# Optimization experiments

Measured on AMD Instinct MI355X. Metric: run time of the kernel, lower is better.

## Reference

```python
import jax, jax.numpy as jnp
import numpy as np

SELF_DIM = 6   # self_state_dim
HID = 50       # lstm_hidden_dim


def setup_inputs() -> dict:
    key = jax.random.key(0)
    ks = jax.random.split(key, 16)
    B, N, D = 8192, 64, 13  # batch, num humans, joint-state length

    def w(k, shape):
        # kaiming-ish init, stored as [in, out] so forward is x @ W + b
        return jax.random.normal(k, shape, jnp.float32) / jnp.sqrt(jnp.float32(shape[0]))

    z = lambda n: jnp.zeros((n,), jnp.float32)
    return {
        "state": jax.random.normal(ks[0], (B, N, D), jnp.float32),
        # mlp1: 13 -> 150 -> 100, last_relu=True
        "mlp1_w1": w(ks[1], (13, 150)),  "mlp1_b1": z(150),
        "mlp1_w2": w(ks[2], (150, 100)), "mlp1_b2": z(100),
        # attention: 200 -> 100 -> 100 -> 1 (no relu on last)
        "attn_w1": w(ks[3], (200, 100)), "attn_b1": z(100),
        "attn_w2": w(ks[4], (100, 100)), "attn_b2": z(100),
        "attn_w3": w(ks[5], (100, 1)),   "attn_b3": z(1),
        # LSTM(input=7, hidden=50), torch gate order i,f,g,o
        "lstm_wih": w(ks[6], (7, 4 * HID)),
        "lstm_whh": w(ks[7], (HID, 4 * HID)),
        "lstm_bih": z(4 * HID), "lstm_bhh": z(4 * HID),
        # mlp: 56 -> 150 -> 100 -> 100 -> 1
        "mlp_w1": w(ks[8], (SELF_DIM + HID, 150)), "mlp_b1": z(150),
        "mlp_w2": w(ks[9], (150, 100)),            "mlp_b2": z(100),
        "mlp_w3": w(ks[10], (100, 100)),           "mlp_b3": z(100),
        "mlp_w4": w(ks[11], (100, 1)),             "mlp_b4": z(1),
    }


def reference(state, mlp1_w1, mlp1_b1, mlp1_w2, mlp1_b2,
              attn_w1, attn_b1, attn_w2, attn_b2, attn_w3, attn_b3,
              lstm_wih, lstm_whh, lstm_bih, lstm_bhh,
              mlp_w1, mlp_b1, mlp_w2, mlp_b2, mlp_w3, mlp_b3, mlp_w4, mlp_b4):
    relu = jax.nn.relu
    B, N, D = state.shape
    self_state = state[:, 0, :SELF_DIM]      # [B, 6]
    human_state = state[:, :, SELF_DIM:]     # [B, N, 7]

    # mlp1 over all B*N per-human joint-state rows (last_relu=True)
    flat = state.reshape(B * N, D)
    m1 = relu(relu(flat @ mlp1_w1 + mlp1_b1) @ mlp1_w2 + mlp1_b2)   # [B*N, 100]

    # mean-pooled global state, broadcast back per human, concat, attention score
    gdim = m1.shape[-1]
    global_state = jnp.mean(m1.reshape(B, N, gdim), axis=1, keepdims=True)
    global_state = jnp.broadcast_to(global_state, (B, N, gdim)).reshape(B * N, gdim)
    a_in = jnp.concatenate([m1, global_state], axis=1)               # [B*N, 200]
    scores = (relu(relu(a_in @ attn_w1 + attn_b1) @ attn_w2 + attn_b2) @ attn_w3 + attn_b3)
    scores = scores.reshape(B, N)
    # NOTE: in the original torch code `scores` only feed `rerank_human_state`,
    # which is never consumed (dead code) -- the LSTM runs on the UNSORTED
    # human_state. We keep the score computation for fidelity; the per-sample
    # argsort/gather is dropped since it does not affect the output.

    # LSTM over the N humans (batch_first in torch, h0=c0=0)
    xs = jnp.transpose(human_state, (1, 0, 2))   # [N, B, 7]
    h0 = jnp.zeros((B, HID), state.dtype)

    def step(carry, x_t):
        h, c = carry
        gates = x_t @ lstm_wih + h @ lstm_whh + lstm_bih + lstm_bhh  # [B, 4H]
        i, f, g, o = jnp.split(gates, 4, axis=-1)
        c = jax.nn.sigmoid(f) * c + jax.nn.sigmoid(i) * jnp.tanh(g)
        h = jax.nn.sigmoid(o) * jnp.tanh(c)
        return (h, c), None

    (hn, _cn), _ = jax.lax.scan(step, (h0, h0), xs)

    # value head on [self_state, h_n]
    joint = jnp.concatenate([self_state, hn], axis=1)   # [B, 56]
    x = relu(joint @ mlp_w1 + mlp_b1)
    x = relu(x @ mlp_w2 + mlp_b2)
    x = relu(x @ mlp_w3 + mlp_b3)
    value = x @ mlp_w4 + mlp_b4                          # [B, 1]
    return value
```

## Files before the change

### kernel.cpp

```cpp
#include <hip/hip_runtime.h>

typedef __attribute__((ext_vector_type(8))) short short8;
typedef __attribute__((ext_vector_type(4))) float f32x4;
union frag_u { short8 v; unsigned short u[8]; };

__device__ __forceinline__ float bf2f(unsigned short b) {
  unsigned int u = ((unsigned int)b) << 16;
  float f; __builtin_memcpy(&f, &u, 4); return f;
}
__device__ __forceinline__ unsigned short f2bf(float f) {
  unsigned int u; __builtin_memcpy(&u, &f, 4);
  return (unsigned short)((u + 0x7FFFu + ((u >> 16) & 1u)) >> 16);
}
__device__ __forceinline__ unsigned short hi_of(float f) { return f2bf(f); }
__device__ __forceinline__ unsigned short lo_of(float f) {
  unsigned short h = f2bf(f); return f2bf(f - bf2f(h));
}
__device__ __forceinline__ float sigm(float x) {
  return __builtin_amdgcn_rcpf(1.f + __expf(-x));
}
__device__ __forceinline__ float tanh_(float x) {
  return 1.f - 2.f * __builtin_amdgcn_rcpf(1.f + __expf(2.f * x));
}

__global__ void detect_dtype_kernel(const unsigned short* s, int* flag) {
  int i = threadIdx.x;
  unsigned short v = s[2 * i];
  int e = (v >> 7) & 0xFF;
  unsigned long long m = __ballot(e < 100 || e > 140);
  if (i == 0) *flag = (__popcll(m) >= 16) ? 1 : 0;
}

template <int AS, typename GetB, typename GetW>
__device__ __forceinline__ void mfma_layer(const unsigned short* sA, float* sG,
    int wave, int col, int quad, int kc_n, int ntiles, int N, GetB getb, GetW getw)
{
  for (int tile = wave; tile < ntiles; tile += 16) {
    int n = tile * 16 + col;
    float b = (n < N) ? getb(n) : 0.f;
    f32x4 acc = {b, b, b, b};
    for (int kc = 0; kc < kc_n; ++kc) {
      short8 a = *(const short8*)&sA[col * AS + kc * 32 + quad * 8];
      frag_u w;
      #pragma unroll
      for (int j = 0; j < 8; ++j) {
        int k = kc * 32 + quad * 8 + j;
        w.u[j] = (n < N) ? getw(k, n) : (unsigned short)0;
      }
      acc = __builtin_amdgcn_mfma_f32_16x16x32_bf16(a, w.v, acc, 0, 0, 0);
    }
    *(f32x4*)&sG[n * 20 + quad * 4] = acc;
  }
}

template <int AS, bool LO>
__device__ __forceinline__ void relu_fill(const float* sG, unsigned short* sA,
                                          int tid, int N, int loOff, int Kpad) {
  for (int idx = tid; idx < 16 * Kpad; idx += 1024) {
    int m = idx & 15, n = idx >> 4;
    unsigned short v = 0;
    if (n < N) {
      v = f2bf(fmaxf(sG[n * 20 + m], 0.f));
    } else if (LO && n >= loOff && n < loOff + N) {
      float x = fmaxf(sG[(n - loOff) * 20 + m], 0.f);
      v = lo_of(x);
    }
    sA[m * AS + n] = v;
  }
}

template <bool F32>
__global__ __launch_bounds__(1024, 8) void value_net_kernel(
    const void* state_, const void* wih_, const void* whh_,
    const void* bih_, const void* bhh_,
    const void* w1_, const void* b1_, const void* w2_, const void* b2_,
    const void* w3_, const void* b3_, const void* w4_, const void* b4_,
    void* out_, const int* flag)
{
  if (flag && *flag != (F32 ? 1 : 0)) return;

  constexpr int AS = F32 ? 328 : 168;
  constexpr int KC = F32 ? 6 : 4;

  __shared__ __align__(16) unsigned short sA[2][16 * AS];
  __shared__ __align__(16) float sG[208 * 20];

  const unsigned short* st16 = (const unsigned short*)state_;
  const float*          stf  = (const float*)state_;

  const int tid  = threadIdx.x;
  const int wave = tid >> 6;
  const int lane = tid & 63;
  const int col  = lane & 15;
  const int quad = lane >> 4;
  const int r0   = blockIdx.x * 16;

  {
    unsigned int* a32 = (unsigned int*)&sA[0][0];
    constexpr int ZT = 16 * AS;
    #pragma unroll
    for (int i = 0; i < (ZT + 1023) / 1024; ++i) {
      int idx = tid + i * 1024;
      if (idx < ZT) a32[idx] = 0;
    }
  }

  auto W_lstm = [&](int k, int n) -> unsigned short {
    if constexpr (!F32) {
      const unsigned short* wih = (const unsigned short*)wih_;
      const unsigned short* whh = (const unsigned short*)whh_;
      if (k < 7)   return wih[k * 200 + n];
      if (k < 57)  return whh[(k - 7) * 200 + n];
      if (k < 107) return whh[(k - 57) * 200 + n];
      return (unsigned short)0;
    } else {
      const float* wih = (const float*)wih_;
      const float* whh = (const float*)whh_;
      if (k < 7)   return hi_of(wih[k * 200 + n]);
      if (k < 14)  return hi_of(wih[(k - 7) * 200 + n]);
      if (k < 21)  return lo_of(wih[(k - 14) * 200 + n]);
      if (k < 71)  return hi_of(whh[(k - 21) * 200 + n]);
      if (k < 121) return hi_of(whh[(k - 71) * 200 + n]);
      if (k < 171) return lo_of(whh[(k - 121) * 200 + n]);
      return (unsigned short)0;
    }
  };
  auto ldf = [&](const void* p, int i) -> float {
    if constexpr (F32) return ((const float*)p)[i];
    else               return bf2f(((const unsigned short*)p)[i]);
  };

  const bool hasTile = (wave < 13);
  frag_u wf[KC];
  float  wb = 0.f;
  if (hasTile) {
    int nn = wave * 16 + col;
    int no = (nn < 200) ? ((nn & 3) * 50 + (nn >> 2)) : 0;
    #pragma unroll
    for (int kc = 0; kc < KC; ++kc) {
      #pragma unroll
      for (int j = 0; j < 8; ++j) {
        int k = kc * 32 + quad * 8 + j;
        wf[kc].u[j] = (nn < 200) ? W_lstm(k, no) : (unsigned short)0;
      }
    }
    wb = (nn < 200) ? (ldf(bih_, no) + ldf(bhh_, no)) : 0.f;
  }

  const int  u_   = wave * 4 + quad;
  const bool iact = hasTile && (u_ < 50);
  float c_ = 0.f, hf = 0.f;

  const bool isx = (tid >= 832) && (tid < 944);
  const int  xm = (tid - 832) / 7, xd = (tid - 832) - ((tid - 832) / 7) * 7;
  auto xgidx = [&](int t) -> size_t { return (size_t)(r0 + xm) * 832 + t * 13 + 6 + xd; };
  auto xwrite = [&](unsigned short* sAw, float fv, unsigned short bv) {
    if constexpr (!F32) { sAw[xm * AS + xd] = bv; }
    else {
      unsigned short h = f2bf(fv);
      sAw[xm * AS + xd] = h; sAw[xm * AS + 14 + xd] = h;
      sAw[xm * AS + 7 + xd] = f2bf(fv - bf2f(h));
    }
  };
  unsigned short xv16 = 0; float xvf = 0.f;

  __syncthreads();
  if (isx) {
    if constexpr (!F32) { xwrite(&sA[0][0], 0.f, st16[xgidx(0)]); xv16 = st16[xgidx(1)]; }
    else                { xwrite(&sA[0][0], stf[xgidx(0)], 0);    xvf  = stf[xgidx(1)]; }
  }
  __syncthreads();

  for (int t = 0; t < 64; ++t) {
    const unsigned short* sAr = &sA[t & 1][0];
    unsigned short*       sAw = &sA[(t & 1) ^ 1][0];

    if (hasTile) {
      short8 a[KC];
      #pragma unroll
      for (int kc = 0; kc < KC; ++kc)
        a[kc] = *(const short8*)&sAr[col * AS + kc * 32 + quad * 8];
      f32x4 acc = {wb, wb, wb, wb};
      #pragma unroll
      for (int kc = 0; kc < KC; ++kc)
        acc = __builtin_amdgcn_mfma_f32_16x16x32_bf16(a[kc], wf[kc].v, acc, 0, 0, 0);
      *(f32x4*)&sG[(wave * 16 + col) * 20 + quad * 4] = acc;

      if (iact) {
        int nb = (wave * 16 + quad * 4);
        float gi = sG[(nb + 0) * 20 + col];
        float gf = sG[(nb + 1) * 20 + col];
        float gg = sG[(nb + 2) * 20 + col];
        float go = sG[(nb + 3) * 20 + col];
        float cc = sigm(gf) * c_ + sigm(gi) * tanh_(gg);
        c_ = cc;
        float h = sigm(go) * tanh_(cc);
        if (t < 63) {
          unsigned short hb = f2bf(h);
          unsigned short hl = f2bf(h - bf2f(hb));
          if constexpr (!F32) {
            sAw[col * AS + 7 + u_] = hb; sAw[col * AS + 57 + u_] = hl;
          } else {
            sAw[col * AS + 21 + u_] = hb; sAw[col * AS + 121 + u_] = hb;
            sAw[col * AS + 71 + u_] = hl;
          }
        } else hf = h;
      }
    } else if (isx && t < 63) {
      if constexpr (!F32) xwrite(sAw, 0.f, xv16); else xwrite(sAw, xvf, 0);
      if (t < 62) { if constexpr (!F32) xv16 = st16[xgidx(t + 2)]; else xvf = stf[xgidx(t + 2)]; }
    }
    __syncthreads();
  }

  unsigned short* sA0 = &sA[0][0];
  {
    constexpr int Z0 = F32 ? 112 : 104;
    constexpr int Z1 = F32 ? 192 : 128;
    for (int idx = tid; idx < 16 * (Z1 - Z0); idx += 1024) {
      int m = idx & 15, n = Z0 + (idx >> 4);
      sA0[m * AS + n] = 0;
    }
  }
  __syncthreads();
  if (iact) {
    unsigned short hb = f2bf(hf);
    unsigned short hl = f2bf(hf - bf2f(hb));
    sA0[col * AS + 6 + u_] = hb;
    if constexpr (!F32) sA0[col * AS + 56 + u_] = hl; else sA0[col * AS + 62 + u_] = hl;
  }
  if (tid < 96) {
    int m = tid / 6, d = tid - (tid / 6) * 6;
    if constexpr (!F32) sA0[m * AS + d] = st16[(size_t)(r0 + m) * 832 + d];
    else {
      float f = stf[(size_t)(r0 + m) * 832 + d];
      sA0[m * AS + d] = hi_of(f); sA0[m * AS + 56 + d] = lo_of(f);
    }
  }
  __syncthreads();

  mfma_layer<AS>(sA0, sG, wave, col, quad, 4, 10, 150,
    [&](int n) { return ldf(b1_, n); },
    [&](int k, int n) -> unsigned short {
      if constexpr (!F32) {
        const unsigned short* w1 = (const unsigned short*)w1_;
        if (k < 56)  return w1[k * 150 + n];
        if (k < 106) return w1[(k - 50) * 150 + n];
        return (unsigned short)0;
      } else {
        const float* w1 = (const float*)w1_;
        if (k < 56)  return hi_of(w1[k * 150 + n]);
        if (k < 112) return hi_of(w1[(k - 56) * 150 + n]);
        return (unsigned short)0;
      }
    });
  __syncthreads();
  if constexpr (!F32) relu_fill<AS, false>(sG, sA0, tid, 150, 160, 160);
  else                relu_fill<AS, true >(sG, sA0, tid, 150, 150, 320);
  __syncthreads();

  mfma_layer<AS>(sA0, sG, wave, col, quad, F32 ? 10 : 5, 7, 100,
    [&](int n) { return ldf(b2_, n); },
    [&](int k, int n) -> unsigned short {
      if constexpr (!F32) {
        const unsigned short* w2 = (const unsigned short*)w2_;
        return (k < 150) ? w2[k * 100 + n] : (unsigned short)0;
      } else {
        const float* w2 = (const float*)w2_;
        if (k < 150) return hi_of(w2[k * 100 + n]);
        if (k < 300) return hi_of(w2[(k - 150) * 100 + n]);
        return (unsigned short)0;
      }
    });
  __syncthreads();
  if constexpr (!F32) relu_fill<AS, false>(sG, sA0, tid, 100, 128, 128);
  else                relu_fill<AS, true >(sG, sA0, tid, 100, 100, 224);
  __syncthreads();

  mfma_layer<AS>(sA0, sG, wave, col, quad, F32 ? 7 : 4, 7, 100,
    [&](int n) { return ldf(b3_, n); },
    [&](int k, int n) -> unsigned short {
      if constexpr (!F32) {
        const unsigned short* w3 = (const unsigned short*)w3_;
        return (k < 100) ? w3[k * 100 + n] : (unsigned short)0;
      } else {
        const float* w3 = (const float*)w3_;
        if (k < 100) return hi_of(w3[k * 100 + n]);
        if (k < 200) return hi_of(w3[(k - 100) * 100 + n]);
        return (unsigned short)0;
      }
    });
  __syncthreads();

  if (tid < 256) {
    int m = tid >> 4, j0 = tid & 15;
    float s = 0.f;
    for (int j = j0; j < 100; j += 16)
      s += fmaxf(sG[j * 20 + m], 0.f) * ldf(w4_, j);
    s += __shfl_xor(s, 8); s += __shfl_xor(s, 4);
    s += __shfl_xor(s, 2); s += __shfl_xor(s, 1);
    if (j0 == 0) {
      float v = s + ldf(b4_, 0);
      if constexpr (!F32) ((unsigned short*)out_)[r0 + m] = f2bf(v);
      else                ((float*)out_)[r0 + m] = v;
    }
  }
}

extern "C" void kernel_launch(void* const* d_in, const int* in_sizes, int n_in,
                              void* d_out, int out_size, void* d_ws, size_t ws_size,
                              hipStream_t stream) {
  (void)n_in; (void)out_size;
  const void* state = d_in[0];
  const void* wih = d_in[11]; const void* whh = d_in[12];
  const void* bih = d_in[13]; const void* bhh = d_in[14];
  const void* w1  = d_in[15]; const void* b1  = d_in[16];
  const void* w2  = d_in[17]; const void* b2  = d_in[18];
  const void* w3  = d_in[19]; const void* b3  = d_in[20];
  const void* w4  = d_in[21]; const void* b4  = d_in[22];

  const long long F32B  = 8192LL * 64 * 13 * 4;
  const long long BF16B = 8192LL * 64 * 13 * 2;
  long long sz = in_sizes ? (long long)in_sizes[0] : -1;

  if (sz == F32B) {
    value_net_kernel<true><<<dim3(512), dim3(1024), 0, stream>>>(
        state, wih, whh, bih, bhh, w1, b1, w2, b2, w3, b3, w4, b4, d_out,
        (const int*)nullptr);
  } else if (sz == BF16B) {
    value_net_kernel<false><<<dim3(512), dim3(1024), 0, stream>>>(
        state, wih, whh, bih, bhh, w1, b1, w2, b2, w3, b3, w4, b4, d_out,
        (const int*)nullptr);
  } else if (ws_size >= sizeof(int)) {
    int* flag = (int*)d_ws;
    detect_dtype_kernel<<<dim3(1), dim3(64), 0, stream>>>(
        (const unsigned short*)state, flag);
    value_net_kernel<false><<<dim3(512), dim3(1024), 0, stream>>>(
        state, wih, whh, bih, bhh, w1, b1, w2, b2, w3, b3, w4, b4, d_out, flag);
    value_net_kernel<true><<<dim3(512), dim3(1024), 0, stream>>>(
        state, wih, whh, bih, bhh, w1, b1, w2, b2, w3, b3, w4, b4, d_out, flag);
  } else {
    value_net_kernel<false><<<dim3(512), dim3(1024), 0, stream>>>(
        state, wih, whh, bih, bhh, w1, b1, w2, b2, w3, b3, w4, b4, d_out,
        (const int*)nullptr);
  }
}
```

Baseline: 232.8 us.

## Collapse each block to a single wave running all LSTM gate tiles without barriers

Each block shrinks from 1024 threads to one 64-lane wave. That wave holds all 13 LSTM weight tiles in registers and runs every gate tile and cell update for its 16 rows itself. This removes the per-timestep __syncthreads and the separate input-loader threads; x prefetch and the MLP head now run inside the same wave. The trade-off is that one wave serialises about 13 times more MFMA and activation work per step. Only 512 waves run across the whole GPU, and register pressure rises sharply from the 13xKC weight fragments.

```diff
diff --git a/kernel.cpp b/kernel.cpp
--- a/kernel.cpp
+++ b/kernel.cpp
@@ -31,46 +31,8 @@
   if (i == 0) *flag = (__popcll(m) >= 16) ? 1 : 0;
 }
 
-template <int AS, typename GetB, typename GetW>
-__device__ __forceinline__ void mfma_layer(const unsigned short* sA, float* sG,
-    int wave, int col, int quad, int kc_n, int ntiles, int N, GetB getb, GetW getw)
-{
-  for (int tile = wave; tile < ntiles; tile += 16) {
-    int n = tile * 16 + col;
-    float b = (n < N) ? getb(n) : 0.f;
-    f32x4 acc = {b, b, b, b};
-    for (int kc = 0; kc < kc_n; ++kc) {
-      short8 a = *(const short8*)&sA[col * AS + kc * 32 + quad * 8];
-      frag_u w;
-      #pragma unroll
-      for (int j = 0; j < 8; ++j) {
-        int k = kc * 32 + quad * 8 + j;
-        w.u[j] = (n < N) ? getw(k, n) : (unsigned short)0;
-      }
-      acc = __builtin_amdgcn_mfma_f32_16x16x32_bf16(a, w.v, acc, 0, 0, 0);
-    }
-    *(f32x4*)&sG[n * 20 + quad * 4] = acc;
-  }
-}
-
-template <int AS, bool LO>
-__device__ __forceinline__ void relu_fill(const float* sG, unsigned short* sA,
-                                          int tid, int N, int loOff, int Kpad) {
-  for (int idx = tid; idx < 16 * Kpad; idx += 1024) {
-    int m = idx & 15, n = idx >> 4;
-    unsigned short v = 0;
-    if (n < N) {
-      v = f2bf(fmaxf(sG[n * 20 + m], 0.f));
-    } else if (LO && n >= loOff && n < loOff + N) {
-      float x = fmaxf(sG[(n - loOff) * 20 + m], 0.f);
-      v = lo_of(x);
-    }
-    sA[m * AS + n] = v;
-  }
-}
-
 template <bool F32>
-__global__ __launch_bounds__(1024, 8) void value_net_kernel(
+__global__ __launch_bounds__(64, 1) void value_net_kernel(
     const void* state_, const void* wih_, const void* whh_,
     const void* bih_, const void* bhh_,
     const void* w1_, const void* b1_, const void* w2_, const void* b2_,
@@ -88,21 +50,14 @@
   const unsigned short* st16 = (const unsigned short*)state_;
   const float*          stf  = (const float*)state_;
 
-  const int tid  = threadIdx.x;
-  const int wave = tid >> 6;
-  const int lane = tid & 63;
+  const int lane = threadIdx.x;
   const int col  = lane & 15;
   const int quad = lane >> 4;
   const int r0   = blockIdx.x * 16;
 
   {
     unsigned int* a32 = (unsigned int*)&sA[0][0];
-    constexpr int ZT = 16 * AS;
-    #pragma unroll
-    for (int i = 0; i < (ZT + 1023) / 1024; ++i) {
-      int idx = tid + i * 1024;
-      if (idx < ZT) a32[idx] = 0;
-    }
+    for (int idx = lane; idx < 16 * AS; idx += 64) a32[idx] = 0;
   }
 
   auto W_lstm = [&](int k, int n) -> unsigned short {
@@ -130,31 +85,34 @@
     else               return bf2f(((const unsigned short*)p)[i]);
   };
 
-  const bool hasTile = (wave < 13);
-  frag_u wf[KC];
-  float  wb = 0.f;
-  if (hasTile) {
-    int nn = wave * 16 + col;
+  frag_u wf[13][KC];
+  float  wb[13];
+  #pragma unroll
+  for (int T = 0; T < 13; ++T) {
+    int nn = T * 16 + col;
     int no = (nn < 200) ? ((nn & 3) * 50 + (nn >> 2)) : 0;
     #pragma unroll
-    for (int kc = 0; kc < KC; ++kc) {
+    for (int kc = 0; kc < KC; ++kc)
       #pragma unroll
       for (int j = 0; j < 8; ++j) {
         int k = kc * 32 + quad * 8 + j;
-        wf[kc].u[j] = (nn < 200) ? W_lstm(k, no) : (unsigned short)0;
-      }
-    }
-    wb = (nn < 200) ? (ldf(bih_, no) + ldf(bhh_, no)) : 0.f;
-  }
-
-  const int  u_   = wave * 4 + quad;
-  const bool iact = hasTile && (u_ < 50);
-  float c_ = 0.f, hf = 0.f;
-
-  const bool isx = (tid >= 832) && (tid < 944);
-  const int  xm = (tid - 832) / 7, xd = (tid - 832) - ((tid - 832) / 7) * 7;
-  auto xgidx = [&](int t) -> size_t { return (size_t)(r0 + xm) * 832 + t * 13 + 6 + xd; };
-  auto xwrite = [&](unsigned short* sAw, float fv, unsigned short bv) {
+        wf[T][kc].u[j] = (nn < 200) ? W_lstm(k, no) : (unsigned short)0;
+      }
+    wb[T] = (nn < 200) ? (ldf(bih_, no) + ldf(bhh_, no)) : 0.f;
+  }
+
+  float c_[13], hf[13];
+  #pragma unroll
+  for (int T = 0; T < 13; ++T) { c_[T] = 0.f; hf[T] = 0.f; }
+
+  const int i1 = lane + 64;
+  const bool v1 = i1 < 112;
+  const int xm0 = lane / 7, xd0 = lane - (lane / 7) * 7;
+  const int xm1 = i1 / 7,   xd1 = i1 - (i1 / 7) * 7;
+  auto xg = [&](int t, int xm, int xd) -> size_t {
+    return (size_t)(r0 + xm) * 832 + (size_t)t * 13 + 6 + xd;
+  };
+  auto xput = [&](unsigned short* sAw, int xm, int xd, float fv, unsigned short bv) {
     if constexpr (!F32) { sAw[xm * AS + xd] = bv; }
     else {
       unsigned short h = f2bf(fv);
@@ -162,147 +120,194 @@
       sAw[xm * AS + 7 + xd] = f2bf(fv - bf2f(h));
     }
   };
-  unsigned short xv16 = 0; float xvf = 0.f;
-
-  __syncthreads();
-  if (isx) {
-    if constexpr (!F32) { xwrite(&sA[0][0], 0.f, st16[xgidx(0)]); xv16 = st16[xgidx(1)]; }
-    else                { xwrite(&sA[0][0], stf[xgidx(0)], 0);    xvf  = stf[xgidx(1)]; }
-  }
-  __syncthreads();
+
+  if constexpr (!F32) {
+    xput(&sA[0][0], xm0, xd0, 0.f, st16[xg(0, xm0, xd0)]);
+    if (v1) xput(&sA[0][0], xm1, xd1, 0.f, st16[xg(0, xm1, xd1)]);
+  } else {
+    xput(&sA[0][0], xm0, xd0, stf[xg(0, xm0, xd0)], 0);
+    if (v1) xput(&sA[0][0], xm1, xd1, stf[xg(0, xm1, xd1)], 0);
+  }
 
   for (int t = 0; t < 64; ++t) {
     const unsigned short* sAr = &sA[t & 1][0];
     unsigned short*       sAw = &sA[(t & 1) ^ 1][0];
 
-    if (hasTile) {
-      short8 a[KC];
+    unsigned short xb0 = 0, xb1 = 0; float xf0 = 0.f, xf1 = 0.f;
+    if (t < 63) {
+      if constexpr (!F32) {
+        xb0 = st16[xg(t + 1, xm0, xd0)];
+        if (v1) xb1 = st16[xg(t + 1, xm1, xd1)];
+      } else {
+        xf0 = stf[xg(t + 1, xm0, xd0)];
+        if (v1) xf1 = stf[xg(t + 1, xm1, xd1)];
+      }
+    }
+
+    short8 a[KC];
+    #pragma unroll
+    for (int kc = 0; kc < KC; ++kc)
+      a[kc] = *(const short8*)&sAr[col * AS + kc * 32 + quad * 8];
+
+    #pragma unroll
+    for (int T = 0; T < 13; ++T) {
+      f32x4 acc = {wb[T], wb[T], wb[T], wb[T]};
       #pragma unroll
       for (int kc = 0; kc < KC; ++kc)
-        a[kc] = *(const short8*)&sAr[col * AS + kc * 32 + quad * 8];
-      f32x4 acc = {wb, wb, wb, wb};
-      #pragma unroll
-      for (int kc = 0; kc < KC; ++kc)
-        acc = __builtin_amdgcn_mfma_f32_16x16x32_bf16(a[kc], wf[kc].v, acc, 0, 0, 0);
-      *(f32x4*)&sG[(wave * 16 + col) * 20 + quad * 4] = acc;
-
-      if (iact) {
-        int nb = (wave * 16 + quad * 4);
+        acc = __builtin_amdgcn_mfma_f32_16x16x32_bf16(a[kc], wf[T][kc].v, acc, 0, 0, 0);
+      *(f32x4*)&sG[(T * 16 + col) * 20 + quad * 4] = acc;
+    }
+
+    #pragma unroll
+    for (int T = 0; T < 13; ++T) {
+      if (T < 12 || quad < 2) {
+        int u  = 4 * T + quad;
+        int nb = T * 16 + quad * 4;
         float gi = sG[(nb + 0) * 20 + col];
         float gf = sG[(nb + 1) * 20 + col];
         float gg = sG[(nb + 2) * 20 + col];
         float go = sG[(nb + 3) * 20 + col];
-        float cc = sigm(gf) * c_ + sigm(gi) * tanh_(gg);
-        c_ = cc;
+        float cc = sigm(gf) * c_[T] + sigm(gi) * tanh_(gg);
+        c_[T] = cc;
         float h = sigm(go) * tanh_(cc);
         if (t < 63) {
           unsigned short hb = f2bf(h);
           unsigned short hl = f2bf(h - bf2f(hb));
           if constexpr (!F32) {
-            sAw[col * AS + 7 + u_] = hb; sAw[col * AS + 57 + u_] = hl;
+            sAw[col * AS + 7 + u] = hb; sAw[col * AS + 57 + u] = hl;
           } else {
-            sAw[col * AS + 21 + u_] = hb; sAw[col * AS + 121 + u_] = hb;
-            sAw[col * AS + 71 + u_] = hl;
+            sAw[col * AS + 21 + u] = hb; sAw[col * AS + 121 + u] = hb;
+            sAw[col * AS + 71 + u] = hl;
           }
-        } else hf = h;
-      }
-    } else if (isx && t < 63) {
-      if constexpr (!F32) xwrite(sAw, 0.f, xv16); else xwrite(sAw, xvf, 0);
-      if (t < 62) { if constexpr (!F32) xv16 = st16[xgidx(t + 2)]; else xvf = stf[xgidx(t + 2)]; }
-    }
-    __syncthreads();
+        } else hf[T] = h;
+      }
+    }
+
+    if (t < 63) {
+      if constexpr (!F32) {
+        xput(sAw, xm0, xd0, 0.f, xb0);
+        if (v1) xput(sAw, xm1, xd1, 0.f, xb1);
+      } else {
+        xput(sAw, xm0, xd0, xf0, 0);
+        if (v1) xput(sAw, xm1, xd1, xf1, 0);
+      }
+    }
   }
 
   unsigned short* sA0 = &sA[0][0];
   {
     constexpr int Z0 = F32 ? 112 : 104;
     constexpr int Z1 = F32 ? 192 : 128;
-    for (int idx = tid; idx < 16 * (Z1 - Z0); idx += 1024) {
-      int m = idx & 15, n = Z0 + (idx >> 4);
-      sA0[m * AS + n] = 0;
-    }
-  }
-  __syncthreads();
-  if (iact) {
-    unsigned short hb = f2bf(hf);
-    unsigned short hl = f2bf(hf - bf2f(hb));
-    sA0[col * AS + 6 + u_] = hb;
-    if constexpr (!F32) sA0[col * AS + 56 + u_] = hl; else sA0[col * AS + 62 + u_] = hl;
-  }
-  if (tid < 96) {
-    int m = tid / 6, d = tid - (tid / 6) * 6;
+    for (int idx = lane; idx < 16 * (Z1 - Z0); idx += 64) {
+      int m = idx & 15, n2 = Z0 + (idx >> 4);
+      sA0[m * AS + n2] = 0;
+    }
+  }
+  #pragma unroll
+  for (int T = 0; T < 13; ++T) {
+    if (T < 12 || quad < 2) {
+      int u = 4 * T + quad;
+      unsigned short hb = f2bf(hf[T]);
+      unsigned short hl = f2bf(hf[T] - bf2f(hb));
+      sA0[col * AS + 6 + u] = hb;
+      if constexpr (!F32) sA0[col * AS + 56 + u] = hl;
+      else                sA0[col * AS + 62 + u] = hl;
+    }
+  }
+  for (int idx = lane; idx < 96; idx += 64) {
+    int m = idx / 6, d = idx - (idx / 6) * 6;
     if constexpr (!F32) sA0[m * AS + d] = st16[(size_t)(r0 + m) * 832 + d];
     else {
       float f = stf[(size_t)(r0 + m) * 832 + d];
       sA0[m * AS + d] = hi_of(f); sA0[m * AS + 56 + d] = lo_of(f);
     }
   }
-  __syncthreads();
-
-  mfma_layer<AS>(sA0, sG, wave, col, quad, 4, 10, 150,
-    [&](int n) { return ldf(b1_, n); },
-    [&](int k, int n) -> unsigned short {
+
+  auto layer = [&](int kc_n, int ntiles, int N, auto getb, auto getw) {
+    for (int tile = 0; tile < ntiles; ++tile) {
+      int nn = tile * 16 + col;
+      float b = (nn < N) ? getb(nn) : 0.f;
+      f32x4 acc = {b, b, b, b};
+      for (int kc = 0; kc < kc_n; ++kc) {
+        short8 a = *(const short8*)&sA0[col * AS + kc * 32 + quad * 8];
+        frag_u w;
+        #pragma unroll
+        for (int j = 0; j < 8; ++j) {
+          int k = kc * 32 + quad * 8 + j;
+          w.u[j] = (nn < N) ? getw(k, nn) : (unsigned short)0;
+        }
+        acc = __builtin_amdgcn_mfma_f32_16x16x32_bf16(a, w.v, acc, 0, 0, 0);
+      }
+      *(f32x4*)&sG[nn * 20 + quad * 4] = acc;
+    }
+  };
+  auto refill = [&](int N, int loOff, int Kpad) {
+    for (int idx = lane; idx < 16 * Kpad; idx += 64) {
+      int m = idx & 15, nn = idx >> 4;
+      unsigned short v = 0;
+      if (nn < N) v = f2bf(fmaxf(sG[nn * 20 + m], 0.f));
+      else if (nn >= loOff && nn < loOff + N)
+        v = lo_of(fmaxf(sG[(nn - loOff) * 20 + m], 0.f));
+      sA0[m * AS + nn] = v;
+    }
+  };
+
+  layer(4, 10, 150,
+    [&](int nn) { return ldf(b1_, nn); },
+    [&](int k, int nn) -> unsigned short {
       if constexpr (!F32) {
         const unsigned short* w1 = (const unsigned short*)w1_;
-        if (k < 56)  return w1[k * 150 + n];
-        if (k < 106) return w1[(k - 50) * 150 + n];
+        if (k < 56)  return w1[k * 150 + nn];
+        if (k < 106) return w1[(k - 50) * 150 + nn];
         return (unsigned short)0;
       } else {
         const float* w1 = (const float*)w1_;
-        if (k < 56)  return hi_of(w1[k * 150 + n]);
-        if (k < 112) return hi_of(w1[(k - 56) * 150 + n]);
+        if (k < 56)  return hi_of(w1[k * 150 + nn]);
+        if (k < 112) return hi_of(w1[(k - 56) * 150 + nn]);
         return (unsigned short)0;
       }
     });
-  __syncthreads();
-  if constexpr (!F32) relu_fill<AS, false>(sG, sA0, tid, 150, 160, 160);
-  else                relu_fill<AS, true >(sG, sA0, tid, 150, 150, 320);
-  __syncthreads();
-
-  mfma_layer<AS>(sA0, sG, wave, col, quad, F32 ? 10 : 5, 7, 100,
-    [&](int n) { return ldf(b2_, n); },
-    [&](int k, int n) -> unsigned short {
+  if constexpr (!F32) refill(150, 160, 160); else refill(150, 150, 320);
+
+  layer(F32 ? 10 : 5, 7, 100,
+    [&](int nn) { return ldf(b2_, nn); },
+    [&](int k, int nn) -> unsigned short {
       if constexpr (!F32) {
         const unsigned short* w2 = (const unsigned short*)w2_;
-        return (k < 150) ? w2[k * 100 + n] : (unsigned short)0;
+        return (k < 150) ? w2[k * 100 + nn] : (unsigned short)0;
       } else {
         const float* w2 = (const float*)w2_;
-        if (k < 150) return hi_of(w2[k * 100 + n]);
-        if (k < 300) return hi_of(w2[(k - 150) * 100 + n]);
+        if (k < 150) return hi_of(w2[k * 100 + nn]);
+        if (k < 300) return hi_of(w2[(k - 150) * 100 + nn]);
         return (unsigned short)0;
       }
     });
-  __syncthreads();
-  if constexpr (!F32) relu_fill<AS, false>(sG, sA0, tid, 100, 128, 128);
-  else                relu_fill<AS, true >(sG, sA0, tid, 100, 100, 224);
-  __syncthreads();
-
-  mfma_layer<AS>(sA0, sG, wave, col, quad, F32 ? 7 : 4, 7, 100,
-    [&](int n) { return ldf(b3_, n); },
-    [&](int k, int n) -> unsigned short {
+  if constexpr (!F32) refill(100, 128, 128); else refill(100, 100, 224);
+
+  layer(F32 ? 7 : 4, 7, 100,
+    [&](int nn) { return ldf(b3_, nn); },
+    [&](int k, int nn) -> unsigned short {
       if constexpr (!F32) {
         const unsigned short* w3 = (const unsigned short*)w3_;
-        return (k < 100) ? w3[k * 100 + n] : (unsigned short)0;
+        return (k < 100) ? w3[k * 100 + nn] : (unsigned short)0;
       } else {
         const float* w3 = (const float*)w3_;
-        if (k < 100) return hi_of(w3[k * 100 + n]);
-        if (k < 200) return hi_of(w3[(k - 100) * 100 + n]);
+        if (k < 100) return hi_of(w3[k * 100 + nn]);
+        if (k < 200) return hi_of(w3[(k - 100) * 100 + nn]);
         return (unsigned short)0;
       }
     });
-  __syncthreads();
-
-  if (tid < 256) {
-    int m = tid >> 4, j0 = tid & 15;
+
+  {
     float s = 0.f;
-    for (int j = j0; j < 100; j += 16)
-      s += fmaxf(sG[j * 20 + m], 0.f) * ldf(w4_, j);
-    s += __shfl_xor(s, 8); s += __shfl_xor(s, 4);
-    s += __shfl_xor(s, 2); s += __shfl_xor(s, 1);
-    if (j0 == 0) {
+    for (int j = quad; j < 100; j += 4)
+      s += fmaxf(sG[j * 20 + col], 0.f) * ldf(w4_, j);
+    s += __shfl_xor(s, 16);
+    s += __shfl_xor(s, 32);
+    if (quad == 0) {
       float v = s + ldf(b4_, 0);
-      if constexpr (!F32) ((unsigned short*)out_)[r0 + m] = f2bf(v);
-      else                ((float*)out_)[r0 + m] = v;
+      if constexpr (!F32) ((unsigned short*)out_)[r0 + col] = f2bf(v);
+      else                ((float*)out_)[r0 + col] = v;
     }
   }
 }
@@ -324,23 +329,23 @@
   long long sz = in_sizes ? (long long)in_sizes[0] : -1;
 
   if (sz == F32B) {
-    value_net_kernel<true><<<dim3(512), dim3(1024), 0, stream>>>(
+    value_net_kernel<true><<<dim3(512), dim3(64), 0, stream>>>(
         state, wih, whh, bih, bhh, w1, b1, w2, b2, w3, b3, w4, b4, d_out,
         (const int*)nullptr);
   } else if (sz == BF16B) {
-    value_net_kernel<false><<<dim3(512), dim3(1024), 0, stream>>>(
+    value_net_kernel<false><<<dim3(512), dim3(64), 0, stream>>>(
         state, wih, whh, bih, bhh, w1, b1, w2, b2, w3, b3, w4, b4, d_out,
         (const int*)nullptr);
   } else if (ws_size >= sizeof(int)) {
     int* flag = (int*)d_ws;
     detect_dtype_kernel<<<dim3(1), dim3(64), 0, stream>>>(
         (const unsigned short*)state, flag);
-    value_net_kernel<false><<<dim3(512), dim3(1024), 0, stream>>>(
+    value_net_kernel<false><<<dim3(512), dim3(64), 0, stream>>>(
         state, wih, whh, bih, bhh, w1, b1, w2, b2, w3, b3, w4, b4, d_out, flag);
-    value_net_kernel<true><<<dim3(512), dim3(1024), 0, stream>>>(
+    value_net_kernel<true><<<dim3(512), dim3(64), 0, stream>>>(
         state, wih, whh, bih, bhh, w1, b1, w2, b2, w3, b3, w4, b4, d_out, flag);
   } else {
-    value_net_kernel<false><<<dim3(512), dim3(1024), 0, stream>>>(
+    value_net_kernel<false><<<dim3(512), dim3(64), 0, stream>>>(
         state, wih, whh, bih, bhh, w1, b1, w2, b2, w3, b3, w4, b4, d_out,
         (const int*)nullptr);
   }
```

New measurement: 657.8 us. 183% more time.
